# Optimization experiments

Measured on AMD Instinct MI355X. Metric: run time of the kernel, lower is better.

## Reference

```python
import jax, jax.numpy as jnp
import numpy as np
import math

IN_F = 1024
OUT_F = 1024
B = 16
L = 4096  # img_size (number of positions)


def setup_inputs() -> dict:
    key = jax.random.key(0)
    k1, k2, k3 = jax.random.split(key, 3)
    Efou = jax.random.normal(k1, (B, L, IN_F), dtype=jnp.float32)
    y = jax.random.normal(k2, (B, IN_F), dtype=jnp.float32)
    weight = jax.random.normal(k3, (1, OUT_F, IN_F, 1), dtype=jnp.float32)
    return {"Efou": Efou, "y": y, "weight": weight}


def reference(Efou, y, weight):
    b, img_size, in_f = Efou.shape
    out_f = weight.shape[1]
    scale = 1.0 / math.sqrt(in_f)
    # per-sample modulated weights: [B, out, in]
    w = scale * weight[:, :, :, 0] * y[:, None, :]
    # demodulation norm over the input-feature axis
    dnorm = jax.lax.rsqrt(jnp.sum(w * w, axis=2, keepdims=True) + 1e-8)  # [B, out, 1]
    w = w * dnorm
    # faithful to torch: Efou.reshape(1, B*in, L) is a raw row-major reshape
    E = Efou.reshape(b, in_f, img_size)  # [B, in, L] (same bytes as original)
    x = jnp.einsum('boi,bil->bol', w, E)  # grouped conv1d, kernel size 1
    # faithful to torch: x.view(B, L, out) is a raw reshape of [B, out, L]
    return x.reshape(b, img_size, out_f)
```

## Files before the change

### kernel.cpp

```cpp
#include <hip/hip_runtime.h>
#include <hip/hip_bf16.h>
#include <cstdint>
#include <cstddef>

typedef __bf16 bf16x8 __attribute__((ext_vector_type(8)));
typedef __bf16 bf16x4 __attribute__((ext_vector_type(4)));
typedef float f32x4 __attribute__((ext_vector_type(4)));

#define BATCH 16
#define MDIM 1024
#define NDIM 4096
#define KDIM 1024
#define BM 256
#define BN 256
#define BK 64
#define NKT (KDIM / BK)

__device__ __forceinline__ void gload_lds16(const void* g, void* l) {
  __builtin_amdgcn_global_load_lds(
      (const __attribute__((address_space(1))) void*)g,
      (__attribute__((address_space(3))) void*)l, 16, 0, 0);
}

#define BAR() __builtin_amdgcn_s_barrier()
#define SB() __builtin_amdgcn_sched_barrier(0)
#define LGKM0()                                        \
  do {                                                 \
    asm volatile("s_waitcnt lgkmcnt(0)" ::: "memory"); \
    SB();                                              \
  } while (0)
#define VMC32()                                        \
  do {                                                 \
    asm volatile("s_waitcnt vmcnt(32)" ::: "memory");  \
    SB();                                              \
  } while (0)

__global__ __launch_bounds__(256) void modw_kernel(
    const float* __restrict__ weight, const float* __restrict__ y,
    __bf16* __restrict__ wm) {
  const int blk = blockIdx.x;
  const int b = blk & 15;
  const int o = blk >> 4;
  const int t = threadIdx.x;
  const float4 w4 = reinterpret_cast<const float4*>(weight + (size_t)o * KDIM)[t];
  const float4 y4 = reinterpret_cast<const float4*>(y + (size_t)b * KDIM)[t];
  const float p0 = w4.x * y4.x, p1 = w4.y * y4.y;
  const float p2 = w4.z * y4.z, p3 = w4.w * y4.w;
  float s = p0 * p0 + p1 * p1 + p2 * p2 + p3 * p3;
#pragma unroll
  for (int off = 32; off >= 1; off >>= 1) s += __shfl_xor(s, off, 64);
  __shared__ float ps[4];
  if ((t & 63) == 0) ps[t >> 6] = s;
  __syncthreads();
  const float tot = ps[0] + ps[1] + ps[2] + ps[3];
  const float scale = 0.03125f;
  const float dn = scale * rsqrtf(scale * scale * tot + 1e-8f);
  bf16x4 v;
  v[0] = (__bf16)(p0 * dn);
  v[1] = (__bf16)(p1 * dn);
  v[2] = (__bf16)(p2 * dn);
  v[3] = (__bf16)(p3 * dn);
  *reinterpret_cast<bf16x4*>(wm + ((size_t)b * MDIM + o) * KDIM + t * 4) = v;
}

__global__ __launch_bounds__(512, 2) void gemm_kernel(
    const __bf16* __restrict__ Wm, const float* __restrict__ E,
    float* __restrict__ out) {
  const int orig = blockIdx.x;
  const int wg = (orig & 7) * 128 + (orig >> 3);
  const int mt = wg & 3;
  const int nt = (wg >> 2) & 15;
  const int b = wg >> 6;
  const int m0 = mt * BM, n0 = nt * BN;

  __shared__ __align__(16) char smem[131072];
  char* const A0_ = smem;
  char* const A1_ = smem + 32768;
  char* const B0_ = smem + 65536;
  char* const B1_ = smem + 98304;

  const int tid = threadIdx.x;
  const int lane = tid & 63;
  const int wid = tid >> 6;
  const int wr = wid >> 2;
  const int wc = wid & 3;
  const int ml = lane & 15;
  const int kg = lane >> 4;

  const int arow = tid >> 3;
  const int aswz = ((tid & 7) ^ (arow & 7)) * 8;
  const __bf16* Ag = Wm + ((size_t)(b * MDIM + m0 + arow)) * KDIM + aswz;
  const int aldsOff = tid * 16;

  const int bn1 = tid & 63;
  const int bkg = tid >> 6;
  typedef const __attribute__((address_space(1))) float gfloat;
  gfloat* Eg = (gfloat*)(E + (size_t)b * KDIM * NDIM +
                         (size_t)(bkg * 8) * NDIM + n0 + bn1);
  int bwr[4];
#pragma unroll
  for (int c = 0; c < 4; ++c) {
    const int n = bn1 + 64 * c;
    bwr[c] = n * 128 + ((bkg * 16) ^ ((n & 7) << 4));
  }

  const int colA = (kg * 16) ^ ((ml & 7) << 4);
  const int arB = (wr * 128 + ml) * 128;
  const int brB = (wc * 64 + ml) * 128;

  f32x4 acc[8][4];
#pragma unroll
  for (int i = 0; i < 8; ++i)
#pragma unroll
    for (int j = 0; j < 4; ++j) acc[i][j] = (f32x4){0.f, 0.f, 0.f, 0.f};

  auto stageA = [&](char* Ab, int kt) {
#pragma unroll
    for (int r = 0; r < 4; ++r)
      gload_lds16(Ag + (size_t)(64 * r) * KDIM + kt * BK,
                  Ab + aldsOff + r * 8192);
  };
  auto loadB = [&](float (&brr)[4][8], int kt) {
#pragma unroll
    for (int c = 0; c < 4; ++c)
#pragma unroll
      for (int j = 0; j < 8; ++j)
        brr[c][j] = Eg[(size_t)(kt * BK + j) * NDIM + 64 * c];
  };
  auto writeB = [&](char* Bb, float (&brr)[4][8]) {
#pragma unroll
    for (int c = 0; c < 4; ++c) {
      bf16x8 v;
#pragma unroll
      for (int j = 0; j < 8; ++j) v[j] = (__bf16)brr[c][j];
      *reinterpret_cast<bf16x8*>(Bb + bwr[c]) = v;
    }
  };

#define RD_B(Bc, KKv)                                          \
  do {                                                         \
    _Pragma("unroll") for (int nf = 0; nf < 4; ++nf)           \
        bf[nf] = *reinterpret_cast<const bf16x8*>(             \
            (Bc) + brB + nf * 2048 + (colA ^ ((KKv)*64)));     \
  } while (0)
#define RD_A(Ac, QMv, KKv)                                         \
  do {                                                             \
    _Pragma("unroll") for (int i = 0; i < 4; ++i)                  \
        af[i] = *reinterpret_cast<const bf16x8*>(                  \
            (Ac) + arB + ((QMv)*4 + i) * 2048 + (colA ^ ((KKv)*64))); \
  } while (0)
#define MFMA16(QMv)                                                      \
  do {                                                                   \
    __builtin_amdgcn_s_setprio(1);                                       \
    _Pragma("unroll") for (int i = 0; i < 4; ++i)                        \
        _Pragma("unroll") for (int nf = 0; nf < 4; ++nf)                 \
            acc[(QMv)*4 + i][nf] = __builtin_amdgcn_mfma_f32_16x16x32_bf16( \
                af[i], bf[nf], acc[(QMv)*4 + i][nf], 0, 0, 0);           \
    __builtin_amdgcn_s_setprio(0);                                       \
  } while (0)

  float br[4][8];

  {
    float brT[4][8];
    loadB(brT, 0);
    stageA(A0_, 0);
    writeB(B0_, brT);
    loadB(br, 1);
    VMC32();
    LGKM0();
    BAR();
    SB();
  }

#pragma unroll 1
  for (int it = 0; it < NKT / 2; ++it) {
    const int e = 2 * it, o = e + 1;
    const int pe = (e + 2 < NKT) ? e + 2 : 0;
    const int po = (o + 2 < NKT) ? o + 2 : 1;
    bf16x8 af[4], bf[4];

    RD_B(B0_, 0);
    RD_A(A0_, 0, 0);
    stageA(A1_, o);
    BAR();
    LGKM0();
    MFMA16(0);
    BAR();
    SB();
    RD_A(A0_, 1, 0);
    writeB(B1_, br);
    BAR();
    LGKM0();
    MFMA16(1);
    BAR();
    SB();
    RD_B(B0_, 1);
    RD_A(A0_, 0, 1);
    loadB(br, pe);
    BAR();
    LGKM0();
    MFMA16(0);
    BAR();
    SB();
    RD_A(A0_, 1, 1);
    BAR();
    LGKM0();
    MFMA16(1);
    VMC32();
    BAR();
    SB();
    RD_B(B1_, 0);
    RD_A(A1_, 0, 0);
    stageA(A0_, pe);
    BAR();
    LGKM0();
    MFMA16(0);
    BAR();
    SB();
    RD_A(A1_, 1, 0);
    writeB(B0_, br);
    BAR();
    LGKM0();
    MFMA16(1);
    BAR();
    SB();
    RD_B(B1_, 1);
    RD_A(A1_, 0, 1);
    loadB(br, po);
    BAR();
    LGKM0();
    MFMA16(0);
    BAR();
    SB();
    RD_A(A1_, 1, 1);
    BAR();
    LGKM0();
    MFMA16(1);
    VMC32();
    BAR();
    SB();
  }
#undef RD_B
#undef RD_A
#undef MFMA16

  float* ob = out + ((size_t)(b * MDIM + m0 + wr * 128 + kg * 4)) * NDIM +
              n0 + wc * 64 + ml;
#pragma unroll
  for (int mf = 0; mf < 8; ++mf)
#pragma unroll
    for (int nf = 0; nf < 4; ++nf) {
      const f32x4 a = acc[mf][nf];
      float* p = ob + (size_t)mf * 16 * NDIM + nf * 16;
#pragma unroll
      for (int q = 0; q < 4; ++q) p[(size_t)q * NDIM] = a[q];
    }
}

extern "C" void kernel_launch(void* const* d_in, const int* in_sizes, int n_in,
                              void* d_out, int out_size, void* d_ws,
                              size_t ws_size, hipStream_t stream) {
  (void)in_sizes;
  (void)n_in;
  (void)out_size;
  (void)ws_size;
  const float* Efou = (const float*)d_in[0];
  const float* y = (const float*)d_in[1];
  const float* weight = (const float*)d_in[2];
  float* outp = (float*)d_out;
  __bf16* wm = (__bf16*)d_ws;

  modw_kernel<<<dim3(BATCH * MDIM), dim3(256), 0, stream>>>(weight, y, wm);
  gemm_kernel<<<dim3(BATCH * (MDIM / BM) * (NDIM / BN)), dim3(512), 0,
                stream>>>(wm, Efou, outp);
}
```

Measured before the change: 236.2 us.

## Simplify GEMM main loop to one barrier per k-tile with swapped buffers

Replaces the hand-interleaved two-tile loop body with a single-tile loop over rotating LDS buffer pointers. The old body had a barrier around each of eight MFMA groups; the new one has one barrier per k-tile. Each iteration first writes the prefetched B registers and issues the async A stage into the other buffer, then prefetches B two tiles ahead, then runs all MFMAs for the current tile. This cuts barrier and wait overhead, but loses the fine-grained mixing of global loads and LDS writes with MFMA work, and the LDS write of B now sits in front of the compute.

```diff
diff --git a/kernel.cpp b/kernel.cpp
--- a/kernel.cpp
+++ b/kernel.cpp
@@ -24,6 +24,7 @@
 
 #define BAR() __builtin_amdgcn_s_barrier()
 #define SB() __builtin_amdgcn_sched_barrier(0)
+#define FENCE() asm volatile("" ::: "memory")
 #define LGKM0()                                        \
   do {                                                 \
     asm volatile("s_waitcnt lgkmcnt(0)" ::: "memory"); \
@@ -32,6 +33,11 @@
 #define VMC32()                                        \
   do {                                                 \
     asm volatile("s_waitcnt vmcnt(32)" ::: "memory");  \
+    SB();                                              \
+  } while (0)
+#define VMC0()                                         \
+  do {                                                 \
+    asm volatile("s_waitcnt vmcnt(0)" ::: "memory");   \
     SB();                                              \
   } while (0)
 
@@ -137,113 +143,77 @@
     }
   };
 
-#define RD_B(Bc, KKv)                                          \
-  do {                                                         \
-    _Pragma("unroll") for (int nf = 0; nf < 4; ++nf)           \
-        bf[nf] = *reinterpret_cast<const bf16x8*>(             \
-            (Bc) + brB + nf * 2048 + (colA ^ ((KKv)*64)));     \
-  } while (0)
-#define RD_A(Ac, QMv, KKv)                                         \
-  do {                                                             \
-    _Pragma("unroll") for (int i = 0; i < 4; ++i)                  \
-        af[i] = *reinterpret_cast<const bf16x8*>(                  \
-            (Ac) + arB + ((QMv)*4 + i) * 2048 + (colA ^ ((KKv)*64))); \
-  } while (0)
-#define MFMA16(QMv)                                                      \
-  do {                                                                   \
-    __builtin_amdgcn_s_setprio(1);                                       \
-    _Pragma("unroll") for (int i = 0; i < 4; ++i)                        \
-        _Pragma("unroll") for (int nf = 0; nf < 4; ++nf)                 \
-            acc[(QMv)*4 + i][nf] = __builtin_amdgcn_mfma_f32_16x16x32_bf16( \
-                af[i], bf[nf], acc[(QMv)*4 + i][nf], 0, 0, 0);           \
-    __builtin_amdgcn_s_setprio(0);                                       \
-  } while (0)
-
   float br[4][8];
 
   {
     float brT[4][8];
+    stageA(A0_, 0);
+    FENCE();
+    SB();
     loadB(brT, 0);
-    stageA(A0_, 0);
     writeB(B0_, brT);
     loadB(br, 1);
-    VMC32();
     LGKM0();
     BAR();
-    SB();
   }
 
+  char* Ac = A0_;
+  char* Ao = A1_;
+  char* Bc = B0_;
+  char* Bo = B1_;
+
 #pragma unroll 1
-  for (int it = 0; it < NKT / 2; ++it) {
-    const int e = 2 * it, o = e + 1;
-    const int pe = (e + 2 < NKT) ? e + 2 : 0;
-    const int po = (o + 2 < NKT) ? o + 2 : 1;
-    bf16x8 af[4], bf[4];
-
-    RD_B(B0_, 0);
-    RD_A(A0_, 0, 0);
-    stageA(A1_, o);
+  for (int t = 0; t < NKT; ++t) {
+    if (t + 1 < NKT) {
+      writeB(Bo, br);
+      stageA(Ao, t + 1);
+      FENCE();
+      SB();
+    }
+    if (t + 2 < NKT) loadB(br, t + 2);
+
+#pragma unroll
+    for (int kk = 0; kk < 2; ++kk) {
+      const int kx = colA ^ (kk * 64);
+      bf16x8 af[4], bf[4];
+#pragma unroll
+      for (int nf = 0; nf < 4; ++nf)
+        bf[nf] = *reinterpret_cast<const bf16x8*>(Bc + brB + nf * 2048 + kx);
+#pragma unroll
+      for (int i = 0; i < 4; ++i)
+        af[i] = *reinterpret_cast<const bf16x8*>(Ac + arB + i * 2048 + kx);
+      __builtin_amdgcn_s_setprio(1);
+#pragma unroll
+      for (int i = 0; i < 4; ++i)
+#pragma unroll
+        for (int nf = 0; nf < 4; ++nf)
+          acc[i][nf] = __builtin_amdgcn_mfma_f32_16x16x32_bf16(
+              af[i], bf[nf], acc[i][nf], 0, 0, 0);
+      __builtin_amdgcn_s_setprio(0);
+#pragma unroll
+      for (int i = 0; i < 4; ++i)
+        af[i] = *reinterpret_cast<const bf16x8*>(Ac + arB + (4 + i) * 2048 + kx);
+      __builtin_amdgcn_s_setprio(1);
+#pragma unroll
+      for (int i = 0; i < 4; ++i)
+#pragma unroll
+        for (int nf = 0; nf < 4; ++nf)
+          acc[4 + i][nf] = __builtin_amdgcn_mfma_f32_16x16x32_bf16(
+              af[i], bf[nf], acc[4 + i][nf], 0, 0, 0);
+      __builtin_amdgcn_s_setprio(0);
+    }
+
+    if (t + 2 < NKT) {
+      VMC32();
+    } else {
+      VMC0();
+    }
+    LGKM0();
     BAR();
-    LGKM0();
-    MFMA16(0);
-    BAR();
-    SB();
-    RD_A(A0_, 1, 0);
-    writeB(B1_, br);
-    BAR();
-    LGKM0();
-    MFMA16(1);
-    BAR();
-    SB();
-    RD_B(B0_, 1);
-    RD_A(A0_, 0, 1);
-    loadB(br, pe);
-    BAR();
-    LGKM0();
-    MFMA16(0);
-    BAR();
-    SB();
-    RD_A(A0_, 1, 1);
-    BAR();
-    LGKM0();
-    MFMA16(1);
-    VMC32();
-    BAR();
-    SB();
-    RD_B(B1_, 0);
-    RD_A(A1_, 0, 0);
-    stageA(A0_, pe);
-    BAR();
-    LGKM0();
-    MFMA16(0);
-    BAR();
-    SB();
-    RD_A(A1_, 1, 0);
-    writeB(B0_, br);
-    BAR();
-    LGKM0();
-    MFMA16(1);
-    BAR();
-    SB();
-    RD_B(B1_, 1);
-    RD_A(A1_, 0, 1);
-    loadB(br, po);
-    BAR();
-    LGKM0();
-    MFMA16(0);
-    BAR();
-    SB();
-    RD_A(A1_, 1, 1);
-    BAR();
-    LGKM0();
-    MFMA16(1);
-    VMC32();
-    BAR();
-    SB();
+
+    char* ta = Ac; Ac = Ao; Ao = ta;
+    char* tb = Bc; Bc = Bo; Bo = tb;
   }
-#undef RD_B
-#undef RD_A
-#undef MFMA16
 
   float* ob = out + ((size_t)(b * MDIM + m0 + wr * 128 + kg * 4)) * NDIM +
               n0 + wc * 64 + ml;
```

New measurement: 213.3 us. 9.7% less time.
